# Kernel tuning notes

Measured on AMD Instinct MI355X. Metric: run time of the kernel, lower is better.

Reference implementation:

```python
import jax, jax.numpy as jnp
import numpy as np

N, D, K = 131072, 128, 512


def _sq_euclidean(x, c):
    x2 = jnp.sum(x * x, axis=1, keepdims=True)
    c2 = jnp.sum(c * c, axis=1)
    return x2 + c2 - 2.0 * (x @ c.T)


def setup_inputs() -> dict:
    key = jax.random.key(0)
    k1, k2 = jax.random.split(key)
    embedded = jax.random.normal(k1, (N, D), dtype=jnp.float32)
    centers = jax.random.normal(k2, (K, D), dtype=jnp.float32)
    count = jnp.ones((K,), dtype=jnp.int32) * 100  # as in fit()
    return {"embedded": embedded, "centers": centers, "count": count}


def reference(embedded, centers, count):
    dist = _sq_euclidean(embedded, centers)          # [N, K]
    loss = jnp.min(dist, axis=1).mean()              # dcn_loss
    labels = jnp.argmin(dist, axis=1)                # predict_hard

    # Sequential per-sample running-mean centroid update (Eq. 8):
    # count[c] += 1; eta = 1/count[c]; centers[c] = (1-eta)*centers[c] + eta*e
    def step(carry, inp):
        ctrs, cnt = carry
        e, c = inp
        new_cnt_c = cnt[c] + 1
        cnt = cnt.at[c].set(new_cnt_c)
        eta = 1.0 / new_cnt_c.astype(ctrs.dtype)
        ctrs = ctrs.at[c].set((1.0 - eta) * ctrs[c] + eta * e)
        return (ctrs, cnt), None

    (new_centers, new_count), _ = jax.lax.scan(step, (centers, count), (embedded, labels))
    return loss, labels, new_centers, new_count
```

## Files before the change

### kernel.cpp

```cpp
#include <hip/hip_runtime.h>

constexpr int NS = 131072;
constexpr int D  = 128;
constexpr int K  = 512;
constexpr int FLAG_CAP = 32768;
constexpr float TAU = 8e-3f;
constexpr int SEG = 32;
constexpr int NB = 64;
constexpr int ITEMS = NS / NB;
constexpr float FIXSCALE = 1048576.0f;
constexpr double INVFIX  = 1.0 / 1048576.0;

typedef __attribute__((ext_vector_type(8))) short short8;
typedef __attribute__((ext_vector_type(4))) float f32x4;


__device__ inline unsigned short f2bf(float f) {
    unsigned int u = __float_as_uint(f);
    unsigned int r = (u + 0x7FFFu + ((u >> 16) & 1u)) >> 16;
    return (unsigned short)r;
}
__device__ inline float bf2f(unsigned short h) {
    return __uint_as_float(((unsigned int)h) << 16);
}

__global__ void k_prep(const float* __restrict__ C, float* __restrict__ c2,
                       unsigned short* __restrict__ Chi, unsigned short* __restrict__ Clo) {
    int wave = (blockIdx.x * blockDim.x + threadIdx.x) >> 6;
    int lane = threadIdx.x & 63;
    const float* ck = C + (size_t)wave * D;
    float a = ck[lane];
    float b = ck[lane + 64];
    unsigned short ha = f2bf(a), hb = f2bf(b);
    size_t o = (size_t)wave * D + lane;
    Chi[o] = ha;           Clo[o] = f2bf(a - bf2f(ha));
    Chi[o + 64] = hb;      Clo[o + 64] = f2bf(b - bf2f(hb));
    float s = fmaf(a, a, b * b);
    #pragma unroll
    for (int off = 32; off > 0; off >>= 1) s += __shfl_xor(s, off, 64);
    if (lane == 0) c2[wave] = s;
}

__global__ __launch_bounds__(256, 2) void k_dist(
    const float* __restrict__ X, const unsigned short* __restrict__ Chi,
    const unsigned short* __restrict__ Clo, const float* __restrict__ c2,
    float* __restrict__ labF, float* __restrict__ mindist, int* __restrict__ labI,
    int* __restrict__ flags, int* __restrict__ flagCount)
{
    __shared__ unsigned short Ah[64][136];
    __shared__ unsigned short Al[64][136];
    __shared__ float sx2[64];
    __shared__ float red1[4][64];
    __shared__ float red2[4][64];
    __shared__ int   reda[4][64];

    int tid = threadIdx.x;
    int wave = tid >> 6, lane = tid & 63;
    int l15 = lane & 15, lk = lane >> 4;
    int s0 = blockIdx.x * 64;

    {
        int row = tid >> 2, part = tid & 3;
        const float4* src = (const float4*)(X + (size_t)(s0 + row) * D + part * 32);
        float q = 0.f;
        #pragma unroll
        for (int j = 0; j < 8; ++j) {
            float4 v = src[j];
            q = fmaf(v.x, v.x, fmaf(v.y, v.y, fmaf(v.z, v.z, fmaf(v.w, v.w, q))));
            ushort4 h, lo;
            h.x = f2bf(v.x); lo.x = f2bf(v.x - bf2f(h.x));
            h.y = f2bf(v.y); lo.y = f2bf(v.y - bf2f(h.y));
            h.z = f2bf(v.z); lo.z = f2bf(v.z - bf2f(h.z));
            h.w = f2bf(v.w); lo.w = f2bf(v.w - bf2f(h.w));
            *(ushort4*)&Ah[row][part * 32 + j * 4] = h;
            *(ushort4*)&Al[row][part * 32 + j * 4] = lo;
        }
        q += __shfl_xor(q, 1, 64);
        q += __shfl_xor(q, 2, 64);
        if (part == 0) sx2[row] = q;
    }
    __syncthreads();

    short8 xh[4][4], xl[4][4];
    #pragma unroll
    for (int n = 0; n < 4; ++n)
        #pragma unroll
        for (int kk = 0; kk < 4; ++kk) {
            int r2 = n * 16 + l15, c = kk * 32 + lk * 8;
            xh[n][kk] = *(const short8*)&Ah[r2][c];
            xl[n][kk] = *(const short8*)&Al[r2][c];
        }

    float m1[4], m2[4]; int ag[4];
    #pragma unroll
    for (int n = 0; n < 4; ++n) { m1[n] = 3.4e38f; m2[n] = 3.4e38f; ag[n] = 0; }

    for (int chunk = 0; chunk < 8; ++chunk) {
        int cb = chunk * 64 + wave * 16;
        const unsigned short* pch = Chi + (size_t)(cb + l15) * D + lk * 8;
        const unsigned short* pcl = Clo + (size_t)(cb + l15) * D + lk * 8;
        short8 ah[4], al[4];
        #pragma unroll
        for (int kk = 0; kk < 4; ++kk) {
            ah[kk] = *(const short8*)(pch + kk * 32);
            al[kk] = *(const short8*)(pcl + kk * 32);
        }
        f32x4 acc[4];
        #pragma unroll
        for (int n = 0; n < 4; ++n) acc[n] = (f32x4){0.f, 0.f, 0.f, 0.f};
        #pragma unroll
        for (int kk = 0; kk < 4; ++kk) {
            #pragma unroll
            for (int n = 0; n < 4; ++n)
                acc[n] = __builtin_amdgcn_mfma_f32_16x16x32_bf16(ah[kk], xh[n][kk], acc[n], 0, 0, 0);
            #pragma unroll
            for (int n = 0; n < 4; ++n)
                acc[n] = __builtin_amdgcn_mfma_f32_16x16x32_bf16(ah[kk], xl[n][kk], acc[n], 0, 0, 0);
            #pragma unroll
            for (int n = 0; n < 4; ++n)
                acc[n] = __builtin_amdgcn_mfma_f32_16x16x32_bf16(al[kk], xh[n][kk], acc[n], 0, 0, 0);
        }
        float cc[4];
        #pragma unroll
        for (int r = 0; r < 4; ++r) cc[r] = c2[cb + lk * 4 + r];
        #pragma unroll
        for (int n = 0; n < 4; ++n)
            #pragma unroll
            for (int r = 0; r < 4; ++r) {
                float s = fmaf(-2.f, acc[n][r], cc[r]);
                int ci = cb + lk * 4 + r;
                bool b = s < m1[n];
                m2[n] = b ? m1[n] : fminf(m2[n], s);
                m1[n] = b ? s : m1[n];
                ag[n] = b ? ci : ag[n];
            }
    }

    #pragma unroll
    for (int off = 16; off <= 32; off <<= 1)
        #pragma unroll
        for (int n = 0; n < 4; ++n) {
            float o1 = __shfl_xor(m1[n], off, 64);
            float o2 = __shfl_xor(m2[n], off, 64);
            int   oa = __shfl_xor(ag[n], off, 64);
            bool b = (o1 < m1[n]) || (o1 == m1[n] && oa < ag[n]);
            float lo1 = b ? o1 : m1[n];
            float hi1 = b ? m1[n] : o1;
            m2[n] = fminf(fminf(m2[n], o2), hi1);
            m1[n] = lo1;
            ag[n] = b ? oa : ag[n];
        }
    if (lane < 16) {
        #pragma unroll
        for (int n = 0; n < 4; ++n) {
            red1[wave][n * 16 + l15] = m1[n];
            red2[wave][n * 16 + l15] = m2[n];
            reda[wave][n * 16 + l15] = ag[n];
        }
    }
    __syncthreads();

    if (tid < 64) {
        float M1 = red1[0][tid], M2 = red2[0][tid]; int A = reda[0][tid];
        #pragma unroll
        for (int w = 1; w < 4; ++w) {
            float o1 = red1[w][tid], o2 = red2[w][tid]; int oa = reda[w][tid];
            bool b = (o1 < M1) || (o1 == M1 && oa < A);
            float lo1 = b ? o1 : M1;
            float hi1 = b ? M1 : o1;
            M2 = fminf(fminf(M2, o2), hi1);
            M1 = lo1;
            A = b ? oa : A;
        }
        int i = s0 + tid;
        labF[i] = (float)A;
        labI[i] = A;
        mindist[i] = sx2[tid] + M1;
        if (M2 - M1 < TAU) {
            int p = atomicAdd(flagCount, 1);
            if (p < FLAG_CAP) flags[p] = i;
        }
    }
}

__global__ void k_refine(const float* __restrict__ X, const float* __restrict__ C,
                         const int* __restrict__ flagCount, const int* __restrict__ flags,
                         float* __restrict__ labF, float* __restrict__ mindist,
                         int* __restrict__ labI)
{
    int nf = *flagCount;
    if (nf > FLAG_CAP) nf = FLAG_CAP;
    int lane = threadIdx.x;
    for (int f = blockIdx.x; f < nf; f += gridDim.x) {
        int i = flags[f];
        const float* xr = X + (size_t)i * D;
        double best = 1e300;
        int bestk = K;
        for (int k = lane; k < K; k += 64) {
            const float* ck = C + (size_t)k * D;
            double dot = 0.0, cc = 0.0;
            for (int d = 0; d < D; ++d) {
                double cd = (double)ck[d];
                dot = fma((double)xr[d], cd, dot);
                cc  = fma(cd, cd, cc);
            }
            double s = cc - 2.0 * dot;
            if (s < best) { best = s; bestk = k; }
        }
        #pragma unroll
        for (int off = 32; off > 0; off >>= 1) {
            double ob = __shfl_xor(best, off, 64);
            int okk   = __shfl_xor(bestk, off, 64);
            if (ob < best || (ob == best && okk < bestk)) { best = ob; bestk = okk; }
        }
        if (lane == 0) {
            double xx = 0.0;
            for (int d = 0; d < D; ++d) xx = fma((double)xr[d], (double)xr[d], xx);
            labF[i] = (float)bestk;
            labI[i] = bestk;
            mindist[i] = (float)(xx + best);
        }
    }
}

__global__ void k_loss(const float* __restrict__ mindist, double* __restrict__ lossSum) {
    __shared__ double sh[4];
    double s = 0.0;
    for (int i = blockIdx.x * blockDim.x + threadIdx.x; i < NS; i += gridDim.x * blockDim.x)
        s += (double)mindist[i];
    #pragma unroll
    for (int off = 32; off > 0; off >>= 1) s += __shfl_xor(s, off, 64);
    int wid = threadIdx.x >> 6, lane = threadIdx.x & 63;
    if (lane == 0) sh[wid] = s;
    __syncthreads();
    if (threadIdx.x == 0) {
        double t = (sh[0] + sh[1]) + (sh[2] + sh[3]);
        atomicAdd(lossSum, t);
    }
}

__global__ __launch_bounds__(256) void k_bh(const int* __restrict__ labI,
                                            int* __restrict__ H) {
    __shared__ int h[K];
    for (int c = threadIdx.x; c < K; c += 256) h[c] = 0;
    __syncthreads();
    int base = blockIdx.x * ITEMS;
    #pragma unroll
    for (int it = 0; it < ITEMS / 256; ++it)
        atomicAdd(&h[labI[base + it * 256 + threadIdx.x]], 1);
    __syncthreads();
    for (int c = threadIdx.x; c < K; c += 256) H[blockIdx.x * K + c] = h[c];
}

__global__ void k_sc(int* __restrict__ H, int* __restrict__ counts) {
    __shared__ int sh[K];
    int c = threadIdx.x;
    int run = 0;
    for (int b = 0; b < NB; ++b) { int t = H[b * K + c]; H[b * K + c] = run; run += t; }
    counts[c] = run;
    sh[c] = run;
    __syncthreads();
    int my = run;
    for (int off = 1; off < K; off <<= 1) {
        int v = (c >= off) ? sh[c - off] : 0;
        __syncthreads();
        sh[c] += v;
        __syncthreads();
    }
    int excl = sh[c] - my;
    for (int b = 0; b < NB; ++b) H[b * K + c] += excl;
}

__global__ __launch_bounds__(256) void k_scatter2(const int* __restrict__ labI,
                                                  const int* __restrict__ H,
                                                  int* __restrict__ bucket) {
    __shared__ int cur[K];
    for (int c = threadIdx.x; c < K; c += 256) cur[c] = H[blockIdx.x * K + c];
    __syncthreads();
    int base = blockIdx.x * ITEMS;
    #pragma unroll
    for (int it = 0; it < ITEMS / 256; ++it) {
        int i = base + it * 256 + threadIdx.x;
        int pos = atomicAdd(&cur[labI[i]], 1);
        bucket[pos] = i;
    }
}

__global__ __launch_bounds__(128) void k_sumseg(
    const float* __restrict__ X, const int* __restrict__ labI,
    const int* __restrict__ bucket, unsigned long long* __restrict__ acc)
{
    int d = threadIdx.x;
    int beg = blockIdx.x * SEG;
    long long s = 0;
    int prev = -1;
    for (int j = beg; j < beg + SEG; ++j) {
        int idx = bucket[j];
        int lab = labI[idx];
        if (lab != prev) {
            if (prev >= 0) atomicAdd(&acc[(size_t)prev * D + d], (unsigned long long)s);
            s = 0; prev = lab;
        }
        float v = X[(size_t)idx * D + d];
        s += (long long)__float2int_rn(v * FIXSCALE);
    }
    if (prev >= 0) atomicAdd(&acc[(size_t)prev * D + d], (unsigned long long)s);
}

__global__ void k_avg(const float* __restrict__ C, const int* __restrict__ cnt,
                      const int* __restrict__ counts,
                      const unsigned long long* __restrict__ acc,
                      float* __restrict__ outC, float* __restrict__ outCnt,
                      const double* __restrict__ lossSum, float* __restrict__ outLoss)
{
    int t = blockIdx.x * blockDim.x + threadIdx.x;
    int c = t >> 7, d = t & 127;
    double s = (double)(long long)acc[t] * INVFIX;
    int m = counts[c], n0 = cnt[c];
    double nm = (double)(n0 + m);
    outC[t] = (float)(((double)n0 * (double)C[t] + s) / nm);
    if (d == 0) outCnt[c] = (float)(n0 + m);
    if (t == 0) outLoss[0] = (float)(*lossSum / (double)NS);
}

extern "C" void kernel_launch(void* const* d_in, const int* in_sizes, int n_in,
                              void* d_out, int out_size, void* d_ws, size_t ws_size,
                              hipStream_t stream)
{
    const float* X  = (const float*)d_in[0];
    const float* C  = (const float*)d_in[1];
    const int* cnt  = (const int*)d_in[2];

    float* out     = (float*)d_out;
    float* outLoss = out;
    float* outLab  = out + 1;
    float* outCen  = out + 1 + NS;
    float* outCnt  = out + 1 + NS + (size_t)K * D;

    char* ws = (char*)d_ws;
    double* lossSum = (double*)(ws + 0);
    int* flagCount  = (int*)(ws + 8);
    float* c2       = (float*)(ws + 16);
    int* counts     = (int*)(ws + 2064);
    float* mindist  = (float*)(ws + 8208);
    int* labI       = (int*)(ws + 532496);
    int* flags      = (int*)(ws + 1056784);
    int* H          = (int*)(ws + 1187856);
    int* bucket     = (int*)(ws + 1318928);
    unsigned long long* acc = (unsigned long long*)(ws + 1843216);
    unsigned short* Chi = (unsigned short*)(ws + 2367504);
    unsigned short* Clo = (unsigned short*)(ws + 2498576);

    hipMemsetAsync(d_ws, 0, 16, stream);
    hipMemsetAsync(ws + 1843216, 0, (size_t)K * D * 8, stream);
    k_prep<<<K / 4, 256, 0, stream>>>(C, c2, Chi, Clo);
    k_dist<<<NS / 64, 256, 0, stream>>>(X, Chi, Clo, c2, outLab, mindist, labI, flags, flagCount);
    k_refine<<<2048, 64, 0, stream>>>(X, C, flagCount, flags, outLab, mindist, labI);
    k_loss<<<256, 256, 0, stream>>>(mindist, lossSum);
    k_bh<<<NB, 256, 0, stream>>>(labI, H);
    k_sc<<<1, K, 0, stream>>>(H, counts);
    k_scatter2<<<NB, 256, 0, stream>>>(labI, H, bucket);
    k_sumseg<<<NS / SEG, 128, 0, stream>>>(X, labI, bucket, acc);
    k_avg<<<K * D / 256, 256, 0, stream>>>(C, cnt, counts, acc, outCen, outCnt, lossSum, outLoss);
}
```

Baseline: 167.4 us.

## Use single bf16 MFMA pass with wider refinement margin and fused x2 loss

Replaces the three-term split-bf16 distance GEMM with a single bf16 product, which cuts MFMA work and the Clo traffic. To keep labels exact, the near-tie threshold is raised sharply so many more samples go to the fp64 refine kernel, and the flag buffer capacity is doubled. X is now loaded straight into registers instead of staged through LDS, occupancy is raised, and flag appends use a wave ballot with one atomic per wave. The ||x||^2 term of the loss moves into k_sumseg. The risk is that refine load grows a lot, and any sample past FLAG_CAP or with bf16 error above TAU gets a wrong label.

```diff
diff --git a/kernel.cpp b/kernel.cpp
--- a/kernel.cpp
+++ b/kernel.cpp
@@ -3,8 +3,8 @@
 constexpr int NS = 131072;
 constexpr int D  = 128;
 constexpr int K  = 512;
-constexpr int FLAG_CAP = 32768;
-constexpr float TAU = 8e-3f;
+constexpr int FLAG_CAP = 65536;
+constexpr float TAU = 0.5f;
 constexpr int SEG = 32;
 constexpr int NB = 64;
 constexpr int ITEMS = NS / NB;
@@ -20,36 +20,29 @@
     unsigned int r = (u + 0x7FFFu + ((u >> 16) & 1u)) >> 16;
     return (unsigned short)r;
 }
-__device__ inline float bf2f(unsigned short h) {
-    return __uint_as_float(((unsigned int)h) << 16);
-}
 
 __global__ void k_prep(const float* __restrict__ C, float* __restrict__ c2,
-                       unsigned short* __restrict__ Chi, unsigned short* __restrict__ Clo) {
+                       unsigned short* __restrict__ Chi) {
     int wave = (blockIdx.x * blockDim.x + threadIdx.x) >> 6;
     int lane = threadIdx.x & 63;
     const float* ck = C + (size_t)wave * D;
     float a = ck[lane];
     float b = ck[lane + 64];
-    unsigned short ha = f2bf(a), hb = f2bf(b);
     size_t o = (size_t)wave * D + lane;
-    Chi[o] = ha;           Clo[o] = f2bf(a - bf2f(ha));
-    Chi[o + 64] = hb;      Clo[o + 64] = f2bf(b - bf2f(hb));
+    Chi[o] = f2bf(a);
+    Chi[o + 64] = f2bf(b);
     float s = fmaf(a, a, b * b);
     #pragma unroll
     for (int off = 32; off > 0; off >>= 1) s += __shfl_xor(s, off, 64);
     if (lane == 0) c2[wave] = s;
 }
 
-__global__ __launch_bounds__(256, 2) void k_dist(
+__global__ __launch_bounds__(256, 3) void k_dist(
     const float* __restrict__ X, const unsigned short* __restrict__ Chi,
-    const unsigned short* __restrict__ Clo, const float* __restrict__ c2,
+    const float* __restrict__ c2,
     float* __restrict__ labF, float* __restrict__ mindist, int* __restrict__ labI,
     int* __restrict__ flags, int* __restrict__ flagCount)
 {
-    __shared__ unsigned short Ah[64][136];
-    __shared__ unsigned short Al[64][136];
-    __shared__ float sx2[64];
     __shared__ float red1[4][64];
     __shared__ float red2[4][64];
     __shared__ int   reda[4][64];
@@ -59,67 +52,40 @@
     int l15 = lane & 15, lk = lane >> 4;
     int s0 = blockIdx.x * 64;
 
-    {
-        int row = tid >> 2, part = tid & 3;
-        const float4* src = (const float4*)(X + (size_t)(s0 + row) * D + part * 32);
-        float q = 0.f;
-        #pragma unroll
-        for (int j = 0; j < 8; ++j) {
-            float4 v = src[j];
-            q = fmaf(v.x, v.x, fmaf(v.y, v.y, fmaf(v.z, v.z, fmaf(v.w, v.w, q))));
-            ushort4 h, lo;
-            h.x = f2bf(v.x); lo.x = f2bf(v.x - bf2f(h.x));
-            h.y = f2bf(v.y); lo.y = f2bf(v.y - bf2f(h.y));
-            h.z = f2bf(v.z); lo.z = f2bf(v.z - bf2f(h.z));
-            h.w = f2bf(v.w); lo.w = f2bf(v.w - bf2f(h.w));
-            *(ushort4*)&Ah[row][part * 32 + j * 4] = h;
-            *(ushort4*)&Al[row][part * 32 + j * 4] = lo;
-        }
-        q += __shfl_xor(q, 1, 64);
-        q += __shfl_xor(q, 2, 64);
-        if (part == 0) sx2[row] = q;
-    }
-    __syncthreads();
-
-    short8 xh[4][4], xl[4][4];
+    short8 xh[4][4];
+    const float* xbase = X + (size_t)(s0 + l15) * D + lk * 8;
     #pragma unroll
     for (int n = 0; n < 4; ++n)
         #pragma unroll
         for (int kk = 0; kk < 4; ++kk) {
-            int r2 = n * 16 + l15, c = kk * 32 + lk * 8;
-            xh[n][kk] = *(const short8*)&Ah[r2][c];
-            xl[n][kk] = *(const short8*)&Al[r2][c];
+            const float* p = xbase + (size_t)n * 16 * D + kk * 32;
+            float4 a = *(const float4*)(p);
+            float4 b = *(const float4*)(p + 4);
+            union { short8 s; unsigned short u[8]; } f;
+            f.u[0] = f2bf(a.x); f.u[1] = f2bf(a.y); f.u[2] = f2bf(a.z); f.u[3] = f2bf(a.w);
+            f.u[4] = f2bf(b.x); f.u[5] = f2bf(b.y); f.u[6] = f2bf(b.z); f.u[7] = f2bf(b.w);
+            xh[n][kk] = f.s;
         }
 
     float m1[4], m2[4]; int ag[4];
     #pragma unroll
     for (int n = 0; n < 4; ++n) { m1[n] = 3.4e38f; m2[n] = 3.4e38f; ag[n] = 0; }
 
+    #pragma unroll 2
     for (int chunk = 0; chunk < 8; ++chunk) {
         int cb = chunk * 64 + wave * 16;
         const unsigned short* pch = Chi + (size_t)(cb + l15) * D + lk * 8;
-        const unsigned short* pcl = Clo + (size_t)(cb + l15) * D + lk * 8;
-        short8 ah[4], al[4];
-        #pragma unroll
-        for (int kk = 0; kk < 4; ++kk) {
-            ah[kk] = *(const short8*)(pch + kk * 32);
-            al[kk] = *(const short8*)(pcl + kk * 32);
-        }
+        short8 ah[4];
+        #pragma unroll
+        for (int kk = 0; kk < 4; ++kk) ah[kk] = *(const short8*)(pch + kk * 32);
         f32x4 acc[4];
         #pragma unroll
         for (int n = 0; n < 4; ++n) acc[n] = (f32x4){0.f, 0.f, 0.f, 0.f};
         #pragma unroll
-        for (int kk = 0; kk < 4; ++kk) {
+        for (int kk = 0; kk < 4; ++kk)
             #pragma unroll
             for (int n = 0; n < 4; ++n)
                 acc[n] = __builtin_amdgcn_mfma_f32_16x16x32_bf16(ah[kk], xh[n][kk], acc[n], 0, 0, 0);
-            #pragma unroll
-            for (int n = 0; n < 4; ++n)
-                acc[n] = __builtin_amdgcn_mfma_f32_16x16x32_bf16(ah[kk], xl[n][kk], acc[n], 0, 0, 0);
-            #pragma unroll
-            for (int n = 0; n < 4; ++n)
-                acc[n] = __builtin_amdgcn_mfma_f32_16x16x32_bf16(al[kk], xh[n][kk], acc[n], 0, 0, 0);
-        }
         float cc[4];
         #pragma unroll
         for (int r = 0; r < 4; ++r) cc[r] = c2[cb + lk * 4 + r];
@@ -175,10 +141,16 @@
         int i = s0 + tid;
         labF[i] = (float)A;
         labI[i] = A;
-        mindist[i] = sx2[tid] + M1;
-        if (M2 - M1 < TAU) {
-            int p = atomicAdd(flagCount, 1);
-            if (p < FLAG_CAP) flags[p] = i;
+        mindist[i] = M1;
+        bool fl = (M2 - M1 < TAU);
+        unsigned long long mask = __ballot(fl);
+        int nfl = (int)__popcll(mask);
+        int base = 0;
+        if (tid == 0 && nfl) base = atomicAdd(flagCount, nfl);
+        base = __shfl(base, 0, 64);
+        if (fl) {
+            int pos = base + (int)__popcll(mask & ((1ull << tid) - 1ull));
+            if (pos < FLAG_CAP) flags[pos] = i;
         }
     }
 }
@@ -214,11 +186,9 @@
             if (ob < best || (ob == best && okk < bestk)) { best = ob; bestk = okk; }
         }
         if (lane == 0) {
-            double xx = 0.0;
-            for (int d = 0; d < D; ++d) xx = fma((double)xr[d], (double)xr[d], xx);
             labF[i] = (float)bestk;
             labI[i] = bestk;
-            mindist[i] = (float)(xx + best);
+            mindist[i] = (float)best;
         }
     }
 }
@@ -288,11 +258,13 @@
 
 __global__ __launch_bounds__(128) void k_sumseg(
     const float* __restrict__ X, const int* __restrict__ labI,
-    const int* __restrict__ bucket, unsigned long long* __restrict__ acc)
+    const int* __restrict__ bucket, unsigned long long* __restrict__ acc,
+    double* __restrict__ x2Sum)
 {
     int d = threadIdx.x;
     int beg = blockIdx.x * SEG;
     long long s = 0;
+    double s2 = 0.0;
     int prev = -1;
     for (int j = beg; j < beg + SEG; ++j) {
         int idx = bucket[j];
@@ -303,15 +275,24 @@
         }
         float v = X[(size_t)idx * D + d];
         s += (long long)__float2int_rn(v * FIXSCALE);
+        s2 = fma((double)v, (double)v, s2);
     }
     if (prev >= 0) atomicAdd(&acc[(size_t)prev * D + d], (unsigned long long)s);
+    #pragma unroll
+    for (int off = 32; off > 0; off >>= 1) s2 += __shfl_xor(s2, off, 64);
+    __shared__ double shx[2];
+    int wid = d >> 6;
+    if ((d & 63) == 0) shx[wid] = s2;
+    __syncthreads();
+    if (d == 0) atomicAdd(&x2Sum[blockIdx.x & 7], shx[0] + shx[1]);
 }
 
 __global__ void k_avg(const float* __restrict__ C, const int* __restrict__ cnt,
                       const int* __restrict__ counts,
                       const unsigned long long* __restrict__ acc,
                       float* __restrict__ outC, float* __restrict__ outCnt,
-                      const double* __restrict__ lossSum, float* __restrict__ outLoss)
+                      const double* __restrict__ lossSum,
+                      const double* __restrict__ x2Sum, float* __restrict__ outLoss)
 {
     int t = blockIdx.x * blockDim.x + threadIdx.x;
     int c = t >> 7, d = t & 127;
@@ -320,7 +301,12 @@
     double nm = (double)(n0 + m);
     outC[t] = (float)(((double)n0 * (double)C[t] + s) / nm);
     if (d == 0) outCnt[c] = (float)(n0 + m);
-    if (t == 0) outLoss[0] = (float)(*lossSum / (double)NS);
+    if (t == 0) {
+        double x2 = 0.0;
+        #pragma unroll
+        for (int j = 0; j < 8; ++j) x2 += x2Sum[j];
+        outLoss[0] = (float)((*lossSum + x2) / (double)NS);
+    }
 }
 
 extern "C" void kernel_launch(void* const* d_in, const int* in_sizes, int n_in,
@@ -339,27 +325,28 @@
 
     char* ws = (char*)d_ws;
     double* lossSum = (double*)(ws + 0);
-    int* flagCount  = (int*)(ws + 8);
-    float* c2       = (float*)(ws + 16);
-    int* counts     = (int*)(ws + 2064);
-    float* mindist  = (float*)(ws + 8208);
-    int* labI       = (int*)(ws + 532496);
-    int* flags      = (int*)(ws + 1056784);
-    int* H          = (int*)(ws + 1187856);
-    int* bucket     = (int*)(ws + 1318928);
-    unsigned long long* acc = (unsigned long long*)(ws + 1843216);
-    unsigned short* Chi = (unsigned short*)(ws + 2367504);
-    unsigned short* Clo = (unsigned short*)(ws + 2498576);
-
-    hipMemsetAsync(d_ws, 0, 16, stream);
-    hipMemsetAsync(ws + 1843216, 0, (size_t)K * D * 8, stream);
-    k_prep<<<K / 4, 256, 0, stream>>>(C, c2, Chi, Clo);
-    k_dist<<<NS / 64, 256, 0, stream>>>(X, Chi, Clo, c2, outLab, mindist, labI, flags, flagCount);
+    double* x2Sum   = (double*)(ws + 8);
+    int* flagCount  = (int*)(ws + 72);
+    float* c2       = (float*)(ws + 80);
+    int* counts     = (int*)(ws + 2128);
+    float* mindist  = (float*)(ws + 4176);
+    int* labI       = (int*)(ws + 528464);
+    int* flags      = (int*)(ws + 1052752);
+    int* H          = (int*)(ws + 1314896);
+    int* bucket     = (int*)(ws + 1445968);
+    unsigned long long* acc = (unsigned long long*)(ws + 1970256);
+    unsigned short* Chi = (unsigned short*)(ws + 2494544);
+
+    hipMemsetAsync(d_ws, 0, 80, stream);
+    hipMemsetAsync(ws + 1970256, 0, (size_t)K * D * 8, stream);
+    k_prep<<<K / 4, 256, 0, stream>>>(C, c2, Chi);
+    k_dist<<<NS / 64, 256, 0, stream>>>(X, Chi, c2, outLab, mindist, labI, flags, flagCount);
     k_refine<<<2048, 64, 0, stream>>>(X, C, flagCount, flags, outLab, mindist, labI);
     k_loss<<<256, 256, 0, stream>>>(mindist, lossSum);
     k_bh<<<NB, 256, 0, stream>>>(labI, H);
     k_sc<<<1, K, 0, stream>>>(H, counts);
     k_scatter2<<<NB, 256, 0, stream>>>(labI, H, bucket);
-    k_sumseg<<<NS / SEG, 128, 0, stream>>>(X, labI, bucket, acc);
-    k_avg<<<K * D / 256, 256, 0, stream>>>(C, cnt, counts, acc, outCen, outCnt, lossSum, outLoss);
-}
+    k_sumseg<<<NS / SEG, 128, 0, stream>>>(X, labI, bucket, acc, x2Sum);
+    k_avg<<<K * D / 256, 256, 0, stream>>>(C, cnt, counts, acc, outCen, outCnt,
+                                           lossSum, x2Sum, outLoss);
+}
```

Result: slower. 426.2 us (+154.6%).
